# Performance work log

Hardware: AMD Instinct MI355X
Metric: run time of the kernel (lower is better)

Reference implementation:

```python
import jax, jax.numpy as jnp
import numpy as np

# Asymmetric NF4 lookup table: NFQuantizer.create_normal_map(offset=0.9677083, num_bits=4)
NF4_TABLE = jnp.array([
    -1.0, -0.6961928009986877, -0.5250730514526367, -0.39491748809814453,
    -0.28444138169288635, -0.18477343022823334, -0.09105003625154495, 0.0,
    0.07958029955625534, 0.16093020141124725, 0.24611230194568634,
    0.33791524171829224, 0.44070982933044434, 0.5626170039176941,
    0.7229568362236023, 1.0], dtype=jnp.float32)

OUT_FEATURES = 4096
IN_FEATURES = 4096
BLOCK_SIZE = 64
NUM_BITS = 4

def setup_inputs() -> dict:
    key = jax.random.key(0)
    k1, k2, k3, k4, k5 = jax.random.split(key, 5)
    n_packed = OUT_FEATURES * IN_FEATURES // (8 // NUM_BITS)      # 8388608
    n_blocks = OUT_FEATURES * IN_FEATURES // BLOCK_SIZE            # 262144
    return {
        "input": jax.random.normal(k1, (2, 1024, IN_FEATURES), dtype=jnp.float32),
        "qweight": jax.random.randint(k2, (n_packed, 1), 0, 256, dtype=jnp.int32),
        "absmax": jax.random.uniform(k3, (n_blocks, 1), dtype=jnp.float32, minval=0.01, maxval=0.05),
        "lora_A": jax.random.normal(k4, (64, IN_FEATURES), dtype=jnp.float32) * 0.02,
        "lora_B": jax.random.normal(k5, (OUT_FEATURES, 64), dtype=jnp.float32) * 0.02,
    }

def dequantize_block(qweight, absmax):
    q = qweight[:, 0]                         # [N/2] packed bytes (int)
    low = NF4_TABLE[q & 0xF]                  # sub-code i=0 (low nibble first)
    high = NF4_TABLE[(q >> 4) & 0xF]          # sub-code i=1
    w = jnp.stack([low, high], axis=-1)       # [N/2, 2], matches torch column order
    w = w.reshape(-1, BLOCK_SIZE) * absmax    # per-block rescale, absmax [n_blocks,1]
    return w.reshape(OUT_FEATURES, IN_FEATURES)

def reference(input, qweight, absmax, lora_A, lora_B):
    weight = dequantize_block(qweight, absmax)          # [out, in] fp32
    ret = input @ weight.T                              # [B, S, out]
    lora = (input @ lora_A.T) @ lora_B.T                # low-rank path
    return ret + lora
```

## Files before the change

### kernel.cpp

```cpp
#include <hip/hip_runtime.h>
#include <hip/hip_bf16.h>
#include <stdint.h>

#define M_DIM 2048
#define N_DIM 4096
#define K_DIM 4096

typedef __attribute__((ext_vector_type(8))) __bf16 bf16x8;
typedef __attribute__((ext_vector_type(4))) float f32x4;

__device__ __constant__ float NF4_TAB[16] = {
    -1.0f, -0.6961928009986877f, -0.5250730514526367f, -0.39491748809814453f,
    -0.28444138169288635f, -0.18477343022823334f, -0.09105003625154495f, 0.0f,
    0.07958029955625534f, 0.16093020141124725f, 0.24611230194568634f,
    0.33791524171829224f, 0.44070982933044434f, 0.5626170039176941f,
    0.7229568362236023f, 1.0f};

__device__ inline unsigned short f2b(float f) {
  union { float f; uint32_t u; } v; v.f = f;
  uint32_t u = v.u;
  return (unsigned short)((u + 0x7fffu + ((u >> 16) & 1u)) >> 16);
}

__global__ void k_cvt(const float4* __restrict__ in, ushort4* __restrict__ out, int n) {
  int i = blockIdx.x * 256 + threadIdx.x;
  if (i < n) {
    float4 v = in[i];
    ushort4 o;
    o.x = f2b(v.x); o.y = f2b(v.y); o.z = f2b(v.z); o.w = f2b(v.w);
    out[i] = o;
  }
}

__global__ void __launch_bounds__(256) k_build_w(
    const int* __restrict__ qw, const float* __restrict__ am,
    const float* __restrict__ lA, const float* __restrict__ lB,
    unsigned short* __restrict__ W) {
  __shared__ float As[64][68];
  __shared__ float BsT[64][68];
  __shared__ float tab[16];
  const int t = threadIdx.x;
  const int bk = blockIdx.x & 63;
  const int bn = blockIdx.x >> 6;
  const int n0 = bn << 6, k0 = bk << 6;
  if (t < 16) tab[t] = NF4_TAB[t];
#pragma unroll
  for (int i = 0; i < 16; ++i) {
    int idx = i * 256 + t;
    int p = idx >> 6, q = idx & 63;
    As[p][q]  = lA[(size_t)p * K_DIM + k0 + q];
    BsT[q][p] = lB[(size_t)(n0 + p) * 64 + q];
  }
  __syncthreads();
  const int tx = t & 15, ty = t >> 4;
  float acc[4][4] = {};
#pragma unroll 8
  for (int r = 0; r < 64; ++r) {
    float4 av = *(const float4*)&As[r][tx * 4];
    float4 bv = *(const float4*)&BsT[r][ty * 4];
    float aa[4] = {av.x, av.y, av.z, av.w};
    float bb[4] = {bv.x, bv.y, bv.z, bv.w};
#pragma unroll
    for (int i = 0; i < 4; ++i)
#pragma unroll
      for (int j = 0; j < 4; ++j) acc[i][j] += bb[i] * aa[j];
  }
#pragma unroll
  for (int i = 0; i < 4; ++i) {
    int row = n0 + ty * 4 + i;
    float amv = am[row * 64 + bk];
    int2 q2 = *(const int2*)&qw[(size_t)row * 2048 + (k0 >> 1) + tx * 2];
    float w0 = tab[q2.x & 15]        * amv + acc[i][0];
    float w1 = tab[(q2.x >> 4) & 15] * amv + acc[i][1];
    float w2 = tab[q2.y & 15]        * amv + acc[i][2];
    float w3 = tab[(q2.y >> 4) & 15] * amv + acc[i][3];
    ushort4 o; o.x = f2b(w0); o.y = f2b(w1); o.z = f2b(w2); o.w = f2b(w3);
    *(ushort4*)&W[(size_t)row * K_DIM + k0 + tx * 4] = o;
  }
}

#define LDSBUF 24576

#define FENCE() asm volatile("" ::: "memory")
#define BAR() do { FENCE(); __builtin_amdgcn_s_barrier(); FENCE(); } while (0)

#define COMPUTE_HALF(QM, BC)                                                     \
  do {                                                                           \
    bf16x8 af[4][2], bv[2][2];                                                   \
    _Pragma("unroll") for (int mi = 0; mi < 4; ++mi) {                           \
      int row = (QM) * 64 + mi * 16 + lr;                                        \
      int rb = row * 64, x = row & 7;                                            \
      _Pragma("unroll") for (int ks = 0; ks < 2; ++ks) {                         \
        int slot = ((ks << 2) | lk) ^ x;                                         \
        af[mi][ks] = *(const bf16x8*)((BC) + rb + slot * 8);                     \
      }                                                                          \
    }                                                                            \
    _Pragma("unroll") for (int ni = 0; ni < 2; ++ni) {                           \
      int row = (wid << 5) + ni * 16 + lr;                                       \
      int rb = 8192 + row * 64, x = row & 7;                                     \
      _Pragma("unroll") for (int ks = 0; ks < 2; ++ks) {                         \
        int slot = ((ks << 2) | lk) ^ x;                                         \
        bv[ni][ks] = *(const bf16x8*)((BC) + rb + slot * 8);                     \
      }                                                                          \
    }                                                                            \
    __builtin_amdgcn_s_setprio(1);                                               \
    _Pragma("unroll") for (int ks = 0; ks < 2; ++ks)                             \
    _Pragma("unroll") for (int mi = 0; mi < 4; ++mi)                             \
    _Pragma("unroll") for (int ni = 0; ni < 2; ++ni)                             \
      acc[(QM) * 4 + mi][ni] = __builtin_amdgcn_mfma_f32_16x16x32_bf16(          \
          af[mi][ks], bv[ni][ks], acc[(QM) * 4 + mi][ni], 0, 0, 0);              \
    __builtin_amdgcn_s_setprio(0);                                               \
  } while (0)

__global__ void __launch_bounds__(512, 2) k_gemm(const unsigned short* __restrict__ A,
                                                 const unsigned short* __restrict__ B,
                                                 float* __restrict__ C) {
  __shared__ unsigned short lds[3 * LDSBUF];
  const int tid = threadIdx.x;
  const int ln = tid & 63;
  const int wid = tid >> 6;
  const int lr = ln & 15;
  const int lk = ln >> 4;

  const int sw = (blockIdx.x & 7) * 32 + (blockIdx.x >> 3);
  const int bm = sw & 15;
  const int bn = sw >> 4;
  const size_t arow0 = (size_t)bm * 128;
  const size_t brow0 = (size_t)bn * 256;

  const int srow = (wid << 3) + (ln >> 3);
  const int gs0 = (ln & 7) ^ (srow & 7);
  auto stage = [&](const unsigned short* __restrict__ G, size_t grow0, int kt,
                   unsigned short* dst) {
    const char* g = (const char*)(G + (grow0 + srow) * (size_t)K_DIM) + kt * 128 + gs0 * 16;
    __builtin_amdgcn_global_load_lds(
        (const __attribute__((address_space(1))) uint32_t*)g,
        (__attribute__((address_space(3))) uint32_t*)(dst + (size_t)(wid << 3) * 64),
        16, 0, 0);
  };

  f32x4 acc[8][2] = {};

  stage(A, arow0, 0, lds);
  stage(A, arow0 + 64, 0, lds + 4096);
  stage(B, brow0, 0, lds + 8192);
  stage(B, brow0 + 64, 0, lds + 12288);
  stage(B, brow0 + 128, 0, lds + 16384);
  stage(B, brow0 + 192, 0, lds + 20480);
  {
    unsigned short* b1 = lds + LDSBUF;
    stage(A, arow0, 1, b1);
    stage(A, arow0 + 64, 1, b1 + 4096);
    stage(B, brow0, 1, b1 + 8192);
    stage(B, brow0 + 64, 1, b1 + 12288);
    stage(B, brow0 + 128, 1, b1 + 16384);
    stage(B, brow0 + 192, 1, b1 + 20480);
  }
  asm volatile("s_waitcnt vmcnt(6)" ::: "memory");
  BAR();

  int cb = 0, sb = 2;
#pragma unroll 1
  for (int t = 0; t < K_DIM / 64; ++t) {
    const unsigned short* bc = lds + cb * LDSBUF;
    unsigned short* sd = lds + sb * LDSBUF;
    int kt2 = t + 2; kt2 = (kt2 >= 64) ? kt2 - 64 : kt2;

    stage(A, arow0, kt2, sd);
    stage(A, arow0 + 64, kt2, sd + 4096);
    stage(B, brow0, kt2, sd + 8192);
    COMPUTE_HALF(0, bc);
    BAR();

    stage(B, brow0 + 64, kt2, sd + 12288);
    stage(B, brow0 + 128, kt2, sd + 16384);
    stage(B, brow0 + 192, kt2, sd + 20480);
    COMPUTE_HALF(1, bc);
    asm volatile("s_waitcnt vmcnt(6)" ::: "memory");
    BAR();

    cb = (cb == 2) ? 0 : cb + 1;
    sb = (sb == 2) ? 0 : sb + 1;
  }

  float* Cb = C + arow0 * N_DIM + brow0 + (wid << 5);
#pragma unroll
  for (int mi8 = 0; mi8 < 8; ++mi8)
#pragma unroll
    for (int ni = 0; ni < 2; ++ni)
#pragma unroll
      for (int r = 0; r < 4; ++r)
        Cb[(size_t)(mi8 * 16 + lk * 4 + r) * N_DIM + ni * 16 + lr] = acc[mi8][ni][r];
}

extern "C" void kernel_launch(void* const* d_in, const int* in_sizes, int n_in,
                              void* d_out, int out_size, void* d_ws, size_t ws_size,
                              hipStream_t stream) {
  const float* input  = (const float*)d_in[0];
  const int* qweight  = (const int*)d_in[1];
  const float* absmax = (const float*)d_in[2];
  const float* lora_A = (const float*)d_in[3];
  const float* lora_B = (const float*)d_in[4];
  float* out = (float*)d_out;

  unsigned short* A16 = (unsigned short*)d_ws;
  unsigned short* B16 = A16 + (size_t)M_DIM * K_DIM;

  int n4 = M_DIM * K_DIM / 4;
  k_cvt<<<n4 / 256, 256, 0, stream>>>((const float4*)input, (ushort4*)A16, n4);
  k_build_w<<<(N_DIM / 64) * (K_DIM / 64), 256, 0, stream>>>(qweight, absmax, lora_A,
                                                             lora_B, B16);
  k_gemm<<<256, 512, 0, stream>>>(A16, B16, out);
}
```

Before: 117.4 us.

## Remap GEMM waves to a 2x4 grid of 64x64 tiles

Each of the 8 waves in the block previously computed a 128x32 output slice. They now form a 2x4 grid and each computes a 64x64 slice. The two compute phases per iteration now split the 64-wide k tile into halves instead of splitting rows of M. This cuts the LDS fragment reads per wave per k tile from 24 to 16 for the same number of MFMAs, which lowers LDS bandwidth pressure. Register use and the output write pattern change shape, which could affect occupancy or the store pattern.

New measurement: 115.9 us. No clear change (-1.3%).

```diff
diff --git a/kernel.cpp b/kernel.cpp
--- a/kernel.cpp
+++ b/kernel.cpp
@@ -84,31 +84,24 @@
 #define FENCE() asm volatile("" ::: "memory")
 #define BAR() do { FENCE(); __builtin_amdgcn_s_barrier(); FENCE(); } while (0)
 
-#define COMPUTE_HALF(QM, BC)                                                     \
+#define COMPUTE_PHASE(KS, BC)                                                    \
   do {                                                                           \
-    bf16x8 af[4][2], bv[2][2];                                                   \
+    bf16x8 af[4], bv[4];                                                         \
     _Pragma("unroll") for (int mi = 0; mi < 4; ++mi) {                           \
-      int row = (QM) * 64 + mi * 16 + lr;                                        \
-      int rb = row * 64, x = row & 7;                                            \
-      _Pragma("unroll") for (int ks = 0; ks < 2; ++ks) {                         \
-        int slot = ((ks << 2) | lk) ^ x;                                         \
-        af[mi][ks] = *(const bf16x8*)((BC) + rb + slot * 8);                     \
-      }                                                                          \
+      int row = wr * 64 + mi * 16 + lr;                                          \
+      int slot = (((KS) << 2) | lk) ^ (row & 7);                                 \
+      af[mi] = *(const bf16x8*)((BC) + row * 64 + slot * 8);                     \
     }                                                                            \
-    _Pragma("unroll") for (int ni = 0; ni < 2; ++ni) {                           \
-      int row = (wid << 5) + ni * 16 + lr;                                       \
-      int rb = 8192 + row * 64, x = row & 7;                                     \
-      _Pragma("unroll") for (int ks = 0; ks < 2; ++ks) {                         \
-        int slot = ((ks << 2) | lk) ^ x;                                         \
-        bv[ni][ks] = *(const bf16x8*)((BC) + rb + slot * 8);                     \
-      }                                                                          \
+    _Pragma("unroll") for (int ni = 0; ni < 4; ++ni) {                           \
+      int row = wc * 64 + ni * 16 + lr;                                          \
+      int slot = (((KS) << 2) | lk) ^ (row & 7);                                 \
+      bv[ni] = *(const bf16x8*)((BC) + 8192 + row * 64 + slot * 8);              \
     }                                                                            \
     __builtin_amdgcn_s_setprio(1);                                               \
-    _Pragma("unroll") for (int ks = 0; ks < 2; ++ks)                             \
     _Pragma("unroll") for (int mi = 0; mi < 4; ++mi)                             \
-    _Pragma("unroll") for (int ni = 0; ni < 2; ++ni)                             \
-      acc[(QM) * 4 + mi][ni] = __builtin_amdgcn_mfma_f32_16x16x32_bf16(          \
-          af[mi][ks], bv[ni][ks], acc[(QM) * 4 + mi][ni], 0, 0, 0);              \
+    _Pragma("unroll") for (int ni = 0; ni < 4; ++ni)                             \
+      acc[mi][ni] = __builtin_amdgcn_mfma_f32_16x16x32_bf16(                     \
+          af[mi], bv[ni], acc[mi][ni], 0, 0, 0);                                 \
     __builtin_amdgcn_s_setprio(0);                                               \
   } while (0)
 
@@ -119,6 +112,8 @@
   const int tid = threadIdx.x;
   const int ln = tid & 63;
   const int wid = tid >> 6;
+  const int wr = wid >> 2;
+  const int wc = wid & 3;
   const int lr = ln & 15;
   const int lk = ln >> 4;
 
@@ -139,7 +134,7 @@
         16, 0, 0);
   };
 
-  f32x4 acc[8][2] = {};
+  f32x4 acc[4][4] = {};
 
   stage(A, arow0, 0, lds);
   stage(A, arow0 + 64, 0, lds + 4096);
@@ -169,13 +164,13 @@
     stage(A, arow0, kt2, sd);
     stage(A, arow0 + 64, kt2, sd + 4096);
     stage(B, brow0, kt2, sd + 8192);
-    COMPUTE_HALF(0, bc);
+    COMPUTE_PHASE(0, bc);
     BAR();
 
     stage(B, brow0 + 64, kt2, sd + 12288);
     stage(B, brow0 + 128, kt2, sd + 16384);
     stage(B, brow0 + 192, kt2, sd + 20480);
-    COMPUTE_HALF(1, bc);
+    COMPUTE_PHASE(1, bc);
     asm volatile("s_waitcnt vmcnt(6)" ::: "memory");
     BAR();
 
@@ -183,14 +178,14 @@
     sb = (sb == 2) ? 0 : sb + 1;
   }
 
-  float* Cb = C + arow0 * N_DIM + brow0 + (wid << 5);
-#pragma unroll
-  for (int mi8 = 0; mi8 < 8; ++mi8)
-#pragma unroll
-    for (int ni = 0; ni < 2; ++ni)
+  float* Cb = C + (arow0 + (size_t)wr * 64) * N_DIM + brow0 + wc * 64;
+#pragma unroll
+  for (int mi = 0; mi < 4; ++mi)
+#pragma unroll
+    for (int ni = 0; ni < 4; ++ni)
 #pragma unroll
       for (int r = 0; r < 4; ++r)
-        Cb[(size_t)(mi8 * 16 + lk * 4 + r) * N_DIM + ni * 16 + lr] = acc[mi8][ni][r];
+        Cb[(size_t)(mi * 16 + lk * 4 + r) * N_DIM + ni * 16 + lr] = acc[mi][ni][r];
 }
 
 extern "C" void kernel_launch(void* const* d_in, const int* in_sizes, int n_in,
```
